# Kernel optimization log

Measured on AMD Instinct MI355X. Metric: run time of the kernel, lower is better.

Reference implementation:

```python
import jax, jax.numpy as jnp
import numpy as np

L, D, H, FF, T, B = 8, 1024, 16, 4096, 2048, 2
HD = D // H
EPS_NORM = 1e-5
EPS_LN = 1e-5


def setup_inputs() -> dict:
    key = jax.random.key(0)
    ks = jax.random.split(key, 8)
    s = 0.02
    return {
        "q": jax.random.normal(ks[0], (B, T, D), jnp.float32),
        "pos_emb": jax.random.uniform(ks[1], (T, D), jnp.float32, -0.05, 0.05),
        "Wqkv": jax.random.normal(ks[2], (L, 3 * D, D), jnp.float32) * s,
        "conv_w": 1.0 + jax.random.normal(ks[3], (L, 3 * D), jnp.float32) * s,
        "proj_w": jax.random.normal(ks[4], (L, D, D), jnp.float32) * s,
        "fc_w": jax.random.normal(ks[5], (L, FF, D), jnp.float32) * s,
        "mlp_w": jax.random.normal(ks[6], (L, D, FF), jnp.float32) * s,
        "gamma": jnp.ones((D,), jnp.float32),
    }


def _l2norm(x):
    # torch F.normalize: x / clamp_min(||x||_2, eps)
    n = jnp.sqrt(jnp.sum(x * x, axis=-1, keepdims=True))
    return x / jnp.maximum(n, EPS_NORM)


def _block(x, Wqkv_i, conv_i, proj_i, fc_i, mlp_i):
    Bb, Tt, _ = x.shape
    # W_qkv linear followed by depthwise 1x1 conv == per-channel scale
    qkv = jnp.einsum("btd,ed->bte", x, Wqkv_i) * conv_i  # [B,T,3D]
    qh, kh, vh = jnp.split(qkv, 3, axis=-1)
    qh = qh.reshape(Bb, Tt, H, HD).transpose(0, 2, 1, 3)  # [B,H,T,hd]
    kh = kh.reshape(Bb, Tt, H, HD).transpose(0, 2, 1, 3)
    vh = vh.reshape(Bb, Tt, H, HD).transpose(0, 2, 1, 3)
    qh = _l2norm(qh)
    kh = _l2norm(kh)
    scores = jnp.einsum("bhqd,bhkd->bhqk", qh, kh) / jnp.sqrt(jnp.float32(HD))
    causal = jnp.tril(jnp.ones((Tt, Tt), bool))
    scores = jnp.where(causal, scores, jnp.finfo(scores.dtype).min)
    attn = jax.nn.softmax(scores, axis=-1)
    y = jnp.einsum("bhqk,bhkd->bhqd", attn, vh)
    y = y.transpose(0, 2, 1, 3).reshape(Bb, Tt, D)
    y = jnp.einsum("btd,ed->bte", y, proj_i)
    x = x + y
    h = jax.nn.gelu(jnp.einsum("btd,fd->btf", x, fc_i), approximate=False)
    h = jnp.einsum("btf,df->btd", h, mlp_i)
    return x + h


def reference(q, pos_emb, Wqkv, conv_w, proj_w, fc_w, mlp_w, gamma):
    x = q + pos_emb[: q.shape[-2], :]
    for i in range(L):
        x = _block(x, Wqkv[i], conv_w[i], proj_w[i], fc_w[i], mlp_w[i])
    mu = jnp.mean(x, axis=-1, keepdims=True)
    var = jnp.mean(jnp.square(x - mu), axis=-1, keepdims=True)
    return (x - mu) / jnp.sqrt(var + EPS_LN) * gamma
```

## Files before the change

### kernel.cpp

```cpp
#include <hip/hip_runtime.h>
#include <math.h>

typedef unsigned short u16;
typedef unsigned int u32;
typedef __attribute__((ext_vector_type(8))) short s16x8;
typedef __attribute__((ext_vector_type(4))) float f32x4;
typedef __attribute__((ext_vector_type(4))) u16 u16x4;

#define B_ 2
#define T_ 2048
#define D_ 1024
#define H_ 16
#define HD_ 64
#define FF_ 4096
#define L_ 8

__device__ __forceinline__ u16 f2b(float f) {
  u32 u = __builtin_bit_cast(u32, f);
  u += 0x7fffu + ((u >> 16) & 1u);
  return (u16)(u >> 16);
}
__device__ __forceinline__ float b2f(u16 h) {
  u32 u = ((u32)h) << 16;
  return __builtin_bit_cast(float, u);
}

__device__ __forceinline__ void load_lds16(const u16* g, u16* l) {
  __builtin_amdgcn_global_load_lds(
      (const __attribute__((address_space(1))) u32*)g,
      (__attribute__((address_space(3))) u32*)l, 16, 0, 0);
}

__global__ __launch_bounds__(256) void fold_qkv_kernel(
    const float* __restrict__ W, const float* __restrict__ conv, u16* __restrict__ out) {
  size_t idx = ((size_t)blockIdx.x * 256 + threadIdx.x) * 4;
  size_t row = idx >> 10;
  float scale = conv[row];
  f32x4 v = *(const f32x4*)&W[idx];
  u16x4 h;
  h.x = f2b(v.x * scale); h.y = f2b(v.y * scale);
  h.z = f2b(v.z * scale); h.w = f2b(v.w * scale);
  *(u16x4*)&out[idx] = h;
}

__global__ __launch_bounds__(256) void cast_kernel(
    const float* __restrict__ in, u16* __restrict__ out) {
  size_t idx = ((size_t)blockIdx.x * 256 + threadIdx.x) * 4;
  f32x4 v = *(const f32x4*)&in[idx];
  u16x4 h;
  h.x = f2b(v.x); h.y = f2b(v.y); h.z = f2b(v.z); h.w = f2b(v.w);
  *(u16x4*)&out[idx] = h;
}

__global__ __launch_bounds__(256) void posadd_kernel(
    const float* __restrict__ q, const float* __restrict__ pos,
    float* __restrict__ xf, u16* __restrict__ xb) {
  size_t idx = ((size_t)blockIdx.x * 256 + threadIdx.x) * 4;
  size_t td = idx & ((size_t)T_ * D_ - 1);
  f32x4 a = *(const f32x4*)&q[idx];
  f32x4 p = *(const f32x4*)&pos[td];
  f32x4 v = a + p;
  *(f32x4*)&xf[idx] = v;
  u16x4 h;
  h.x = f2b(v.x); h.y = f2b(v.y); h.z = f2b(v.z); h.w = f2b(v.w);
  *(u16x4*)&xb[idx] = h;
}

template <int EPI>
__global__ __launch_bounds__(256, 2) void gemm_bt(
    const u16* __restrict__ A, const u16* __restrict__ Bt,
    float* __restrict__ Cf, u16* __restrict__ Cb,
    const float* __restrict__ resid, int M, int N, int K) {
  __shared__ u16 As[128 * 32];
  __shared__ u16 Bs[128 * 32];
  const int tid = threadIdx.x;
  const int lane = tid & 63;
  const int w = tid >> 6;
  const int wr = w >> 1, wc = w & 1;
  const size_t row0 = (size_t)blockIdx.y * 128;
  const size_t col0 = (size_t)blockIdx.x * 128;

  const u16* Ag = A + row0 * K;
  const u16* Bg = Bt + col0 * K;

  f32x4 zero = {0.f, 0.f, 0.f, 0.f};
  f32x4 acc[4][4];
#pragma unroll
  for (int m = 0; m < 4; ++m)
#pragma unroll
    for (int n = 0; n < 4; ++n) acc[m][n] = zero;

  const int chunk0 = w * 2, chunk1 = w * 2 + 1;
  const int e0 = chunk0 * 512 + lane * 8;
  const int e1 = chunk1 * 512 + lane * 8;
  const int r0 = e0 >> 5, c0 = e0 & 31;
  const int r1 = e1 >> 5, c1 = e1 & 31;

  const int fr = lane & 15;
  const int koff = (lane >> 4) * 8;

  for (int k0 = 0; k0 < K; k0 += 32) {
    __syncthreads();
    load_lds16(Ag + (size_t)r0 * K + k0 + c0, &As[chunk0 * 512]);
    load_lds16(Ag + (size_t)r1 * K + k0 + c1, &As[chunk1 * 512]);
    load_lds16(Bg + (size_t)r0 * K + k0 + c0, &Bs[chunk0 * 512]);
    load_lds16(Bg + (size_t)r1 * K + k0 + c1, &Bs[chunk1 * 512]);
    __syncthreads();

    s16x8 a[4], b[4];
#pragma unroll
    for (int m = 0; m < 4; ++m)
      a[m] = *(const s16x8*)&As[(wr * 64 + m * 16 + fr) * 32 + koff];
#pragma unroll
    for (int n = 0; n < 4; ++n)
      b[n] = *(const s16x8*)&Bs[(wc * 64 + n * 16 + fr) * 32 + koff];
#pragma unroll
    for (int m = 0; m < 4; ++m)
#pragma unroll
      for (int n = 0; n < 4; ++n)
        acc[m][n] = __builtin_amdgcn_mfma_f32_16x16x32_bf16(a[m], b[n], acc[m][n], 0, 0, 0);
  }

  const int rq = (lane >> 4) * 4;
#pragma unroll
  for (int m = 0; m < 4; ++m) {
#pragma unroll
    for (int n = 0; n < 4; ++n) {
      size_t col = col0 + wc * 64 + n * 16 + fr;
#pragma unroll
      for (int r = 0; r < 4; ++r) {
        size_t row = row0 + wr * 64 + m * 16 + rq + r;
        size_t idx = row * (size_t)N + col;
        float v = acc[m][n][r];
        if (EPI == 0) {
          Cf[idx] = v;
        } else if (EPI == 1) {
          float o = resid[idx] + v;
          Cf[idx] = o;
          Cb[idx] = f2b(o);
        } else if (EPI == 2) {
          float g = 0.5f * v * (1.0f + erff(v * 0.70710678118654752f));
          Cb[idx] = f2b(g);
        } else {
          Cb[idx] = f2b(v);
        }
      }
    }
  }
}

__global__ __launch_bounds__(256) void qkvnorm_kernel(
    const u16* __restrict__ qkv, u16* __restrict__ qb, u16* __restrict__ kb,
    u16* __restrict__ vb) {
  int gid = blockIdx.x * 4 + (threadIdx.x >> 6);
  int lane = threadIdx.x & 63;
  int h = gid & (H_ - 1);
  int t = (gid >> 4) & (T_ - 1);
  int b = gid >> 15;
  const u16* base = qkv + ((size_t)(b * T_ + t)) * (3 * D_) + h * HD_;
  float qv = b2f(base[lane]);
  float kv = b2f(base[D_ + lane]);
  u16 vv = base[2 * D_ + lane];
  float qs = qv * qv, ks = kv * kv;
#pragma unroll
  for (int off = 1; off < 64; off <<= 1) {
    qs += __shfl_xor(qs, off);
    ks += __shfl_xor(ks, off);
  }
  float qn = qv / fmaxf(sqrtf(qs), 1e-5f);
  float kn = kv / fmaxf(sqrtf(ks), 1e-5f);
  size_t oi = ((size_t)(b * H_ + h) * T_ + t) * HD_ + lane;
  qb[oi] = f2b(qn);
  kb[oi] = f2b(kn);
  vb[oi] = vv;
}

__global__ __launch_bounds__(256) void vtrans_kernel(
    const u16* __restrict__ vb, u16* __restrict__ vt) {
  __shared__ u16 tile[64 * 72];
  const int bh = blockIdx.y;
  const int t0 = blockIdx.x * 64;
  const int tid = threadIdx.x;
  const u16* src = vb + ((size_t)bh * T_ + t0) * HD_;
#pragma unroll
  for (int it = 0; it < 2; ++it) {
    int e = (tid * 2 + it) * 8;
    int r = e >> 6, c = e & 63;
    s16x8 v = *(const s16x8*)&src[(size_t)r * HD_ + c];
    *(s16x8*)&tile[r * 72 + c] = v;
  }
  __syncthreads();
#pragma unroll
  for (int it = 0; it < 2; ++it) {
    int e = (tid * 2 + it) * 8;
    int d = e >> 6, c = e & 63;
    u16 tmp[8];
#pragma unroll
    for (int j = 0; j < 8; ++j) tmp[j] = tile[(c + j) * 72 + d];
    *(s16x8*)&vt[((size_t)bh * HD_ + d) * T_ + t0 + c] = *(const s16x8*)tmp;
  }
}

__global__ __launch_bounds__(512) void attn_kernel(
    const u16* __restrict__ qg, const u16* __restrict__ kg,
    const u16* __restrict__ vtg, u16* __restrict__ y) {
  __shared__ u16 Ks[64 * 72];
  __shared__ u16 Vt[64 * 72];
  __shared__ u16 Ps[8][16 * 72];

  const int tid = threadIdx.x;
  const int lane = tid & 63;
  const int w = tid >> 6;
  const int qt = blockIdx.x;
  const int bh = blockIdx.y;
  const int b = bh >> 4, hh = bh & 15;

  const u16* Q = qg + ((size_t)bh * T_ + qt * 128) * HD_;
  const u16* Kb = kg + (size_t)bh * T_ * HD_;
  const u16* Vg = vtg + (size_t)bh * HD_ * T_;

  const int fr = lane & 15;
  const int koff = (lane >> 4) * 8;

  s16x8 qf0 = *(const s16x8*)&Q[(w * 16 + fr) * HD_ + koff];
  s16x8 qf1 = *(const s16x8*)&Q[(w * 16 + fr) * HD_ + 32 + koff];

  f32x4 zero = {0.f, 0.f, 0.f, 0.f};
  f32x4 o[4];
#pragma unroll
  for (int n = 0; n < 4; ++n) o[n] = zero;
  float mrow[4] = {-1e30f, -1e30f, -1e30f, -1e30f};
  float lrow[4] = {0.f, 0.f, 0.f, 0.f};

  const int sr = tid >> 3;
  const int sc = (tid & 7) * 8;

  const int ktmax = 2 * qt + 1;
  for (int kt = 0; kt <= ktmax; ++kt) {
    __syncthreads();
    {
      s16x8 kv = *(const s16x8*)&Kb[((size_t)kt * 64 + sr) * HD_ + sc];
      *(s16x8*)&Ks[sr * 72 + sc] = kv;
      s16x8 vv = *(const s16x8*)&Vg[(size_t)sr * T_ + kt * 64 + sc];
      *(s16x8*)&Vt[sr * 72 + sc] = vv;
    }
    __syncthreads();

    f32x4 s[4];
#pragma unroll
    for (int n = 0; n < 4; ++n) {
      s16x8 kf0 = *(const s16x8*)&Ks[(n * 16 + fr) * 72 + koff];
      s16x8 kf1 = *(const s16x8*)&Ks[(n * 16 + fr) * 72 + 32 + koff];
      f32x4 z = zero;
      z = __builtin_amdgcn_mfma_f32_16x16x32_bf16(qf0, kf0, z, 0, 0, 0);
      z = __builtin_amdgcn_mfma_f32_16x16x32_bf16(qf1, kf1, z, 0, 0, 0);
      s[n] = z;
    }

    const int grow_base = qt * 128 + w * 16 + (lane >> 4) * 4;
    const int gcol_base = kt * 64 + fr;
    float p[4][4];
#pragma unroll
    for (int r = 0; r < 4; ++r) {
      float mx = -1e30f;
#pragma unroll
      for (int n = 0; n < 4; ++n) {
        float sv = s[n][r] * 0.125f;
        if (gcol_base + n * 16 > grow_base + r) sv = -1e30f;
        s[n][r] = sv;
        mx = fmaxf(mx, sv);
      }
#pragma unroll
      for (int off = 1; off < 16; off <<= 1) mx = fmaxf(mx, __shfl_xor(mx, off));
      float mnew = fmaxf(mrow[r], mx);
      float sc2 = __expf(mrow[r] - mnew);
      float rs = 0.f;
#pragma unroll
      for (int n = 0; n < 4; ++n) {
        float pv = __expf(s[n][r] - mnew);
        p[n][r] = pv;
        rs += pv;
      }
#pragma unroll
      for (int off = 1; off < 16; off <<= 1) rs += __shfl_xor(rs, off);
      lrow[r] = lrow[r] * sc2 + rs;
      mrow[r] = mnew;
#pragma unroll
      for (int n = 0; n < 4; ++n) o[n][r] *= sc2;
    }

    u16* Pw = &Ps[w][0];
#pragma unroll
    for (int n = 0; n < 4; ++n)
#pragma unroll
      for (int r = 0; r < 4; ++r)
        Pw[((lane >> 4) * 4 + r) * 72 + n * 16 + fr] = f2b(p[n][r]);
    asm volatile("s_waitcnt lgkmcnt(0)" ::: "memory");

    s16x8 pa0 = *(const s16x8*)&Pw[fr * 72 + koff];
    s16x8 pa1 = *(const s16x8*)&Pw[fr * 72 + 32 + koff];
#pragma unroll
    for (int n = 0; n < 4; ++n) {
      s16x8 v0 = *(const s16x8*)&Vt[(n * 16 + fr) * 72 + koff];
      s16x8 v1 = *(const s16x8*)&Vt[(n * 16 + fr) * 72 + 32 + koff];
      o[n] = __builtin_amdgcn_mfma_f32_16x16x32_bf16(pa0, v0, o[n], 0, 0, 0);
      o[n] = __builtin_amdgcn_mfma_f32_16x16x32_bf16(pa1, v1, o[n], 0, 0, 0);
    }
  }

#pragma unroll
  for (int n = 0; n < 4; ++n)
#pragma unroll
    for (int r = 0; r < 4; ++r) {
      int grow = qt * 128 + w * 16 + (lane >> 4) * 4 + r;
      float val = o[n][r] / lrow[r];
      y[((size_t)b * T_ + grow) * D_ + hh * 64 + n * 16 + fr] = f2b(val);
    }
}

__global__ __launch_bounds__(256) void ln_kernel(
    const float* __restrict__ x, const float* __restrict__ gamma,
    float* __restrict__ out) {
  int row = blockIdx.x;
  int tid = threadIdx.x;
  const float* xr = x + (size_t)row * D_;
  f32x4 v = *(const f32x4*)&xr[tid * 4];
  float s = v.x + v.y + v.z + v.w;
  float ss = v.x * v.x + v.y * v.y + v.z * v.z + v.w * v.w;
#pragma unroll
  for (int off = 1; off < 64; off <<= 1) {
    s += __shfl_xor(s, off);
    ss += __shfl_xor(ss, off);
  }
  __shared__ float red[8];
  int w = tid >> 6, lane = tid & 63;
  if (lane == 0) {
    red[w] = s;
    red[4 + w] = ss;
  }
  __syncthreads();
  s = red[0] + red[1] + red[2] + red[3];
  ss = red[4] + red[5] + red[6] + red[7];
  float mu = s * (1.f / D_);
  float var = ss * (1.f / D_) - mu * mu;
  float rstd = rsqrtf(var + 1e-5f);
  f32x4 g = *(const f32x4*)&gamma[tid * 4];
  f32x4 o;
  o.x = (v.x - mu) * rstd * g.x;
  o.y = (v.y - mu) * rstd * g.y;
  o.z = (v.z - mu) * rstd * g.z;
  o.w = (v.w - mu) * rstd * g.w;
  *(f32x4*)&out[(size_t)row * D_ + tid * 4] = o;
}

extern "C" void kernel_launch(void* const* d_in, const int* in_sizes, int n_in,
                              void* d_out, int out_size, void* d_ws, size_t ws_size,
                              hipStream_t stream) {
  (void)in_sizes; (void)n_in; (void)out_size; (void)ws_size;
  const float* q = (const float*)d_in[0];
  const float* pos = (const float*)d_in[1];
  const float* Wqkv = (const float*)d_in[2];
  const float* convw = (const float*)d_in[3];
  const float* projw = (const float*)d_in[4];
  const float* fcw = (const float*)d_in[5];
  const float* mlpw = (const float*)d_in[6];
  const float* gamma = (const float*)d_in[7];
  float* out = (float*)d_out;

  char* ws = (char*)d_ws;
  size_t off = 0;
  auto alloc = [&](size_t bytes) {
    char* p = ws + off;
    off += (bytes + 255) & ~(size_t)255;
    return p;
  };
  const size_t nWq = (size_t)3 * D_ * D_;
  const size_t nPr = (size_t)D_ * D_;
  const size_t nFc = (size_t)FF_ * D_;
  const size_t nMl = (size_t)D_ * FF_;
  const size_t nX = (size_t)B_ * T_ * D_;
  const size_t nQKV = (size_t)B_ * T_ * 3 * D_;
  const size_t nH = (size_t)B_ * T_ * FF_;

  u16* Wqb = (u16*)alloc(nWq * 2);
  u16* Prb = (u16*)alloc(nPr * 2);
  u16* Fcb = (u16*)alloc(nFc * 2);
  u16* Mlb = (u16*)alloc(nMl * 2);
  float* xf = (float*)alloc(nX * 4);
  u16* xb = (u16*)alloc(nX * 2);
  size_t shared_bytes = nH * 2 > nQKV * 2 ? nH * 2 : nQKV * 2;
  u16* qkvb = (u16*)alloc(shared_bytes);
  u16* hb = qkvb;
  u16* qb = (u16*)alloc(nX * 2);
  u16* kb = (u16*)alloc(nX * 2);
  u16* vb = (u16*)alloc(nX * 2);
  u16* vtb = (u16*)alloc(nX * 2);
  u16* yb = (u16*)alloc(nX * 2);

  posadd_kernel<<<nX / 1024, 256, 0, stream>>>(q, pos, xf, xb);

  const int M = B_ * T_;
  for (int l = 0; l < L_; ++l) {
    fold_qkv_kernel<<<nWq / 1024, 256, 0, stream>>>(
        Wqkv + (size_t)l * nWq, convw + (size_t)l * 3 * D_, Wqb);
    cast_kernel<<<nPr / 1024, 256, 0, stream>>>(projw + (size_t)l * nPr, Prb);
    cast_kernel<<<nFc / 1024, 256, 0, stream>>>(fcw + (size_t)l * nFc, Fcb);
    cast_kernel<<<nMl / 1024, 256, 0, stream>>>(mlpw + (size_t)l * nMl, Mlb);

    gemm_bt<3><<<dim3(3 * D_ / 128, M / 128), 256, 0, stream>>>(
        xb, Wqb, nullptr, qkvb, nullptr, M, 3 * D_, D_);
    qkvnorm_kernel<<<(B_ * T_ * H_) / 4, 256, 0, stream>>>(qkvb, qb, kb, vb);
    vtrans_kernel<<<dim3(T_ / 64, B_ * H_), 256, 0, stream>>>(vb, vtb);
    attn_kernel<<<dim3(T_ / 128, B_ * H_), 512, 0, stream>>>(qb, kb, vtb, yb);
    gemm_bt<1><<<dim3(D_ / 128, M / 128), 256, 0, stream>>>(
        yb, Prb, xf, xb, xf, M, D_, D_);
    gemm_bt<2><<<dim3(FF_ / 128, M / 128), 256, 0, stream>>>(
        xb, Fcb, nullptr, hb, nullptr, M, FF_, D_);
    gemm_bt<1><<<dim3(D_ / 128, M / 128), 256, 0, stream>>>(
        hb, Mlb, xf, xb, xf, M, D_, FF_);
  }
  ln_kernel<<<B_ * T_, 256, 0, stream>>>(xf, gamma, out);
}
```

Baseline: 3.006 ms.

## Deepen GEMM K-tile with XOR-swizzled LDS; reverse attention tile order and prefetch K/V

```diff
diff --git a/kernel.cpp b/kernel.cpp
--- a/kernel.cpp
+++ b/kernel.cpp
@@ -71,8 +71,8 @@
     const u16* __restrict__ A, const u16* __restrict__ Bt,
     float* __restrict__ Cf, u16* __restrict__ Cb,
     const float* __restrict__ resid, int M, int N, int K) {
-  __shared__ u16 As[128 * 32];
-  __shared__ u16 Bs[128 * 32];
+  __shared__ u16 As[128 * 64];
+  __shared__ u16 Bs[128 * 64];
   const int tid = threadIdx.x;
   const int lane = tid & 63;
   const int w = tid >> 6;
@@ -90,38 +90,47 @@
 #pragma unroll
     for (int n = 0; n < 4; ++n) acc[m][n] = zero;
 
-  const int chunk0 = w * 2, chunk1 = w * 2 + 1;
-  const int e0 = chunk0 * 512 + lane * 8;
-  const int e1 = chunk1 * 512 + lane * 8;
-  const int r0 = e0 >> 5, c0 = e0 & 31;
-  const int r1 = e1 >> 5, c1 = e1 & 31;
-
+  const int srow = tid >> 3;
+  const int scol8 = tid & 7;
   const int fr = lane & 15;
-  const int koff = (lane >> 4) * 8;
-
-  for (int k0 = 0; k0 < K; k0 += 32) {
+  const int g = lane >> 4;
+  const int koff = g * 8;
+
+  for (int k0 = 0; k0 < K; k0 += 64) {
     __syncthreads();
-    load_lds16(Ag + (size_t)r0 * K + k0 + c0, &As[chunk0 * 512]);
-    load_lds16(Ag + (size_t)r1 * K + k0 + c1, &As[chunk1 * 512]);
-    load_lds16(Bg + (size_t)r0 * K + k0 + c0, &Bs[chunk0 * 512]);
-    load_lds16(Bg + (size_t)r1 * K + k0 + c1, &Bs[chunk1 * 512]);
+#pragma unroll
+    for (int i = 0; i < 4; ++i) {
+      int rd = i * 32 + srow;
+      int sc8 = scol8 ^ (rd & 7);
+      load_lds16(Ag + (size_t)rd * K + k0 + sc8 * 8, &As[i * 2048 + w * 512]);
+      load_lds16(Bg + (size_t)rd * K + k0 + sc8 * 8, &Bs[i * 2048 + w * 512]);
+    }
     __syncthreads();
 
-    s16x8 a[4], b[4];
-#pragma unroll
-    for (int m = 0; m < 4; ++m)
-      a[m] = *(const s16x8*)&As[(wr * 64 + m * 16 + fr) * 32 + koff];
-#pragma unroll
-    for (int n = 0; n < 4; ++n)
-      b[n] = *(const s16x8*)&Bs[(wc * 64 + n * 16 + fr) * 32 + koff];
-#pragma unroll
-    for (int m = 0; m < 4; ++m)
-#pragma unroll
-      for (int n = 0; n < 4; ++n)
-        acc[m][n] = __builtin_amdgcn_mfma_f32_16x16x32_bf16(a[m], b[n], acc[m][n], 0, 0, 0);
-  }
-
-  const int rq = (lane >> 4) * 4;
+#pragma unroll
+    for (int kk = 0; kk < 2; ++kk) {
+      s16x8 a[4], b[4];
+#pragma unroll
+      for (int m = 0; m < 4; ++m) {
+        int ra = wr * 64 + m * 16 + fr;
+        int c8 = (kk * 4 + g) ^ (fr & 7);
+        a[m] = *(const s16x8*)&As[ra * 64 + c8 * 8];
+      }
+#pragma unroll
+      for (int n = 0; n < 4; ++n) {
+        int rb = wc * 64 + n * 16 + fr;
+        int c8 = (kk * 4 + g) ^ (fr & 7);
+        b[n] = *(const s16x8*)&Bs[rb * 64 + c8 * 8];
+      }
+#pragma unroll
+      for (int m = 0; m < 4; ++m)
+#pragma unroll
+        for (int n = 0; n < 4; ++n)
+          acc[m][n] = __builtin_amdgcn_mfma_f32_16x16x32_bf16(a[m], b[n], acc[m][n], 0, 0, 0);
+    }
+  }
+
+  const int rq = g * 4;
 #pragma unroll
   for (int m = 0; m < 4; ++m) {
 #pragma unroll
@@ -139,8 +148,8 @@
           Cf[idx] = o;
           Cb[idx] = f2b(o);
         } else if (EPI == 2) {
-          float g = 0.5f * v * (1.0f + erff(v * 0.70710678118654752f));
-          Cb[idx] = f2b(g);
+          float ge = 0.5f * v * (1.0f + erff(v * 0.70710678118654752f));
+          Cb[idx] = f2b(ge);
         } else {
           Cb[idx] = f2b(v);
         }
@@ -211,7 +220,7 @@
   const int tid = threadIdx.x;
   const int lane = tid & 63;
   const int w = tid >> 6;
-  const int qt = blockIdx.x;
+  const int qt = (T_ / 128 - 1) - blockIdx.x;
   const int bh = blockIdx.y;
   const int b = bh >> 4, hh = bh & 15;
 
@@ -234,17 +243,20 @@
 
   const int sr = tid >> 3;
   const int sc = (tid & 7) * 8;
-
   const int ktmax = 2 * qt + 1;
+
+  s16x8 kv = *(const s16x8*)&Kb[((size_t)sr) * HD_ + sc];
+  s16x8 vv = *(const s16x8*)&Vg[(size_t)sr * T_ + sc];
+
   for (int kt = 0; kt <= ktmax; ++kt) {
     __syncthreads();
-    {
-      s16x8 kv = *(const s16x8*)&Kb[((size_t)kt * 64 + sr) * HD_ + sc];
-      *(s16x8*)&Ks[sr * 72 + sc] = kv;
-      s16x8 vv = *(const s16x8*)&Vg[(size_t)sr * T_ + kt * 64 + sc];
-      *(s16x8*)&Vt[sr * 72 + sc] = vv;
-    }
+    *(s16x8*)&Ks[sr * 72 + sc] = kv;
+    *(s16x8*)&Vt[sr * 72 + sc] = vv;
     __syncthreads();
+    if (kt < ktmax) {
+      kv = *(const s16x8*)&Kb[((size_t)(kt + 1) * 64 + sr) * HD_ + sc];
+      vv = *(const s16x8*)&Vg[(size_t)sr * T_ + (kt + 1) * 64 + sc];
+    }
 
     f32x4 s[4];
 #pragma unroll
```

Result: faster. 2.737 ms (-9.0%).
